# Performance work log

Measured on AMD Instinct MI355X. Metric: run time of the kernel, lower is better.

Reference implementation:

```python
import jax, jax.numpy as jnp
import numpy as np

# Object condensation loss config (matches init_kwargs / HGCalML defaults)
Q_MIN = 0.5
S_B = 1.0
POT_SCALE = 1.0
REP_SCALE = 1.0
BETA_SCALE = 1.0
E_WEIGHT = 1.0
HUBER_DELTA = 2.0
E_DEN_OFFSET = 1.0
K_MAX = 192          # object-id slots per event; id 0 = noise
EPS = 1e-6

B, N = 4, 50000


def setup_inputs() -> dict:
    key = jax.random.key(0)
    k1, k2, k3, k4, k5 = jax.random.split(key, 5)
    return {
        "beta": jax.random.uniform(k1, (B, N, 1), dtype=jnp.float32),
        "ccoords": jax.random.normal(k2, (B, N, 2), dtype=jnp.float32),
        "pred_energy": jax.random.uniform(k3, (B, N, 1), dtype=jnp.float32),
        "true_energy": jax.random.uniform(k4, (B, N, 1), dtype=jnp.float32),
        "truth_idx": jax.random.randint(k5, (B, N), 0, K_MAX, dtype=jnp.int32),
    }


def _per_event(beta, ccoords, pred_e, true_e, tidx):
    # beta: [N,1], ccoords: [N,2], tidx: [N] int (0 = noise)
    beta = jnp.clip(beta[:, 0], 1e-4, 1.0 - 1e-4)            # [N]
    q = jnp.arctanh(beta) ** 2 + Q_MIN                        # charge  [N]

    ids = jnp.arange(K_MAX)
    M = (tidx[:, None] == ids[None, :]) & (ids[None, :] > 0)  # [N,K] membership
    Mf = M.astype(q.dtype)
    obj_valid = jnp.any(M, axis=0)                            # [K]
    vf = obj_valid.astype(q.dtype)

    # condensation point alpha_k = argmax_q over members of object k
    qM = jnp.where(M, q[:, None], -1.0)                       # [N,K]
    idx_alpha = jnp.argmax(qM, axis=0)                        # [K]
    x_alpha = ccoords[idx_alpha]                              # [K,2]
    q_alpha = q[idx_alpha]                                    # [K]
    beta_alpha = beta[idx_alpha]                              # [K]

    # pairwise hit<->condensation-point distances
    d2 = jnp.sum((ccoords[:, None, :] - x_alpha[None, :, :]) ** 2, axis=-1)  # [N,K]

    # attractive potential (members), repulsive hinge (non-members of valid objects)
    att = jnp.sum(d2 * q_alpha[None, :] * Mf, axis=-1)                       # [N]
    dist = jnp.sqrt(d2 + EPS)
    rep = jnp.sum(jnp.maximum(0.0, 1.0 - dist) * q_alpha[None, :]
                  * (1.0 - Mf) * vf[None, :], axis=-1)                       # [N]
    L_V = jnp.mean(q * (POT_SCALE * att + REP_SCALE * rep))

    n_obj = jnp.sum(vf) + EPS
    L_beta = BETA_SCALE * jnp.sum((1.0 - beta_alpha) * vf) / n_obj

    noise = (tidx == 0).astype(q.dtype)
    L_noise = S_B * jnp.sum(beta * noise) / (jnp.sum(noise) + EPS)

    # energy payload loss: relative error, Huber, beta-weighted per object
    ediff = (pred_e[:, 0] - true_e[:, 0]) / (true_e[:, 0] + E_DEN_OFFSET)
    ad = jnp.abs(ediff)
    eh = jnp.where(ad <= HUBER_DELTA, 0.5 * ad ** 2,
                   HUBER_DELTA * (ad - 0.5 * HUBER_DELTA))                   # [N]
    pw = Mf * beta[:, None]                                                  # [N,K]
    per_obj_e = jnp.sum(pw * eh[:, None], axis=0) / (jnp.sum(pw, axis=0) + EPS)
    L_E = E_WEIGHT * jnp.sum(per_obj_e * vf) / n_obj

    return L_V + L_beta + L_noise + L_E


def reference(beta, ccoords, pred_energy, true_energy, truth_idx):
    per_ev = jax.vmap(_per_event)(beta, ccoords, pred_energy, true_energy, truth_idx)
    return jnp.mean(per_ev)
```

## Files before the change

kernel.cpp:

```cpp
#include <hip/hip_runtime.h>
#include <math.h>

#define KM 192
#define EPSF 1e-6f
#define QMIN 0.5f
#define BLKA 256
#define HA 4
#define TILEA (BLKA * HA)
#define BLKM 256
#define TILEM (BLKM * 2)

__device__ __forceinline__ float clipb(float b) {
    return fminf(fmaxf(b, 1e-4f), 1.0f - 1e-4f);
}
__device__ __forceinline__ float fast_atanh(float b) {
    float r = (1.f + b) * __builtin_amdgcn_rcpf(1.f - b);
    return 0.34657359f * __builtin_amdgcn_logf(r);
}

__global__ void __launch_bounds__(BLKA)
k_amax(const float* __restrict__ beta, const int* __restrict__ tidx,
       unsigned long long* __restrict__ pscr, int N, int HBT) {
    const int e = blockIdx.y;
    __shared__ unsigned long long smax[KM];
    for (int k = threadIdx.x; k < KM; k += BLKA) smax[k] = 0ull;
    __syncthreads();
    const size_t base = (size_t)e * N;
    #pragma unroll
    for (int h = 0; h < HA; ++h) {
        int i = blockIdx.x * TILEA + h * BLKA + threadIdx.x;
        if (i < N) {
            int t = tidx[base + i];
            if (t > 0) {
                float bc = clipb(beta[base + i]);
                unsigned long long pack =
                    ((unsigned long long)__float_as_uint(bc) << 32) |
                    (unsigned long long)(unsigned)(N - 1 - i);
                atomicMax(&smax[t], pack);
            }
        }
    }
    __syncthreads();
    unsigned long long* row = pscr + ((size_t)e * HBT + blockIdx.x) * KM;
    for (int k = threadIdx.x; k < KM; k += BLKA) row[k] = smax[k];
}

__global__ void __launch_bounds__(256)
k_alpha(const unsigned long long* __restrict__ pscr, const float* __restrict__ cc,
        float4* __restrict__ alpha, float* __restrict__ abw,
        float* __restrict__ enm, float* __restrict__ eden,
        float* __restrict__ scal, int N, int HBT) {
    const int e = blockIdx.x;
    const int k = threadIdx.x;
    if (k < KM) {
        const unsigned long long* pk = pscr + (size_t)e * HBT * KM + k;
        unsigned long long v = 0ull;
        #pragma unroll 8
        for (int t = 0; t < HBT; ++t) {
            unsigned long long p = pk[(size_t)t * KM];
            if (p > v) v = p;
        }
        float4 a = make_float4(0.f, 0.f, 0.f, 0.f);
        float bw = 0.f;
        if (v) {
            int idx = N - 1 - (int)(unsigned)(v & 0xffffffffull);
            bw = __uint_as_float((unsigned)(v >> 32));
            float at = fast_atanh(bw);
            float2 cp = ((const float2*)cc)[(size_t)e * N + idx];
            a.x = cp.x; a.y = cp.y;
            a.z = fmaf(at, at, QMIN);
        }
        alpha[e * KM + k] = a;
        abw  [e * KM + k] = bw;
    }
    for (int z = threadIdx.x; z < KM; z += 256) {
        enm [e * KM + z] = 0.f;
        eden[e * KM + z] = 0.f;
    }
    if (threadIdx.x < 8) scal[e * 8 + threadIdx.x] = 0.f;
}

__global__ void __launch_bounds__(BLKM, 4)
k_main(const float* __restrict__ beta, const float* __restrict__ cc,
       const float* __restrict__ pe,   const float* __restrict__ te,
       const int* __restrict__ tidx,   const float4* __restrict__ alpha,
       float* __restrict__ enm, float* __restrict__ eden,
       float* __restrict__ scal, int N) {
    const int e = blockIdx.y;
    __shared__ float sn[KM], sd[KM];
    __shared__ float sw[12];
    for (int k = threadIdx.x; k < KM; k += BLKM) { sn[k] = 0.f; sd[k] = 0.f; }
    __syncthreads();

    const size_t base = (size_t)e * N;
    const int ia = blockIdx.x * TILEM + threadIdx.x;
    const int ib = ia + BLKM;
    const bool oka = ia < N, okb = ib < N;
    const size_t iia = base + (oka ? ia : 0);
    const size_t iib = base + (okb ? ib : 0);
    const float2 ca = ((const float2*)cc)[iia];
    const float2 cb = ((const float2*)cc)[iib];
    const float bca = clipb(beta[iia]);
    const float bcb = clipb(beta[iib]);
    const int   ta  = oka ? tidx[iia] : 0;
    const int   tb  = okb ? tidx[iib] : 0;
    const float ha_ = fast_atanh(bca);
    const float hb_ = fast_atanh(bcb);
    const float qa  = oka ? fmaf(ha_, ha_, QMIN) : 0.f;
    const float qb  = okb ? fmaf(hb_, hb_, QMIN) : 0.f;

    const float4* __restrict__ ae = alpha + e * KM;
    float ra0 = 0.f, ra1 = 0.f, rb0 = 0.f, rb1 = 0.f;
    #pragma unroll 8
    for (int k = 0; k < KM; k += 2) {
        float4 a0 = ae[k], a1 = ae[k + 1];
        float dxa0 = ca.x - a0.x, dya0 = ca.y - a0.y;
        float dxa1 = ca.x - a1.x, dya1 = ca.y - a1.y;
        float dxb0 = cb.x - a0.x, dyb0 = cb.y - a0.y;
        float dxb1 = cb.x - a1.x, dyb1 = cb.y - a1.y;
        float da0 = fmaf(dxa0, dxa0, fmaf(dya0, dya0, EPSF));
        float da1 = fmaf(dxa1, dxa1, fmaf(dya1, dya1, EPSF));
        float db0 = fmaf(dxb0, dxb0, fmaf(dyb0, dyb0, EPSF));
        float db1 = fmaf(dxb1, dxb1, fmaf(dyb1, dyb1, EPSF));
        ra0 = fmaf(fmaxf(1.f - __builtin_amdgcn_sqrtf(da0), 0.f), a0.z, ra0);
        ra1 = fmaf(fmaxf(1.f - __builtin_amdgcn_sqrtf(da1), 0.f), a1.z, ra1);
        rb0 = fmaf(fmaxf(1.f - __builtin_amdgcn_sqrtf(db0), 0.f), a0.z, rb0);
        rb1 = fmaf(fmaxf(1.f - __builtin_amdgcn_sqrtf(db1), 0.f), a1.z, rb1);
    }
    float repa = ra0 + ra1, repb = rb0 + rb1;
    float atta = 0.f, attb = 0.f, bn = 0.f, cn = 0.f;

    if (ta > 0) {
        float4 av = ae[ta];
        float dx = ca.x - av.x, dy = ca.y - av.y;
        float d2 = fmaf(dx, dx, dy * dy);
        atta = d2 * av.z;
        repa -= fmaxf(1.f - __builtin_amdgcn_sqrtf(d2 + EPSF), 0.f) * av.z;
        float tev = te[iia];
        float edv = (pe[iia] - tev) * __builtin_amdgcn_rcpf(tev + 1.f);
        float ad  = fabsf(edv);
        float eh  = (ad <= 2.f) ? 0.5f * ad * ad : 2.f * (ad - 1.f);
        atomicAdd(&sn[ta], bca * eh);
        atomicAdd(&sd[ta], bca);
    } else if (oka) { bn += bca; cn += 1.f; }

    if (tb > 0) {
        float4 av = ae[tb];
        float dx = cb.x - av.x, dy = cb.y - av.y;
        float d2 = fmaf(dx, dx, dy * dy);
        attb = d2 * av.z;
        repb -= fmaxf(1.f - __builtin_amdgcn_sqrtf(d2 + EPSF), 0.f) * av.z;
        float tev = te[iib];
        float edv = (pe[iib] - tev) * __builtin_amdgcn_rcpf(tev + 1.f);
        float ad  = fabsf(edv);
        float eh  = (ad <= 2.f) ? 0.5f * ad * ad : 2.f * (ad - 1.f);
        atomicAdd(&sn[tb], bcb * eh);
        atomicAdd(&sd[tb], bcb);
    } else if (okb) { bn += bcb; cn += 1.f; }

    float lv = fmaf(qa, atta + repa, qb * (attb + repb));
    __syncthreads();

    if (threadIdx.x < KM) {
        float vd = sd[threadIdx.x];
        if (vd != 0.f) {
            atomicAdd(&enm [e * KM + threadIdx.x], sn[threadIdx.x]);
            atomicAdd(&eden[e * KM + threadIdx.x], vd);
        }
    }
    for (int off = 32; off > 0; off >>= 1) {
        lv += __shfl_down(lv, off);
        bn += __shfl_down(bn, off);
        cn += __shfl_down(cn, off);
    }
    const int wid = threadIdx.x >> 6;
    if ((threadIdx.x & 63) == 0) { sw[wid] = lv; sw[4 + wid] = bn; sw[8 + wid] = cn; }
    __syncthreads();
    if (threadIdx.x == 0) {
        atomicAdd(&scal[e * 8 + 0], (sw[0] + sw[1]) + (sw[2] + sw[3]));
        atomicAdd(&scal[e * 8 + 3], (sw[4] + sw[5]) + (sw[6] + sw[7]));
        atomicAdd(&scal[e * 8 + 4], (sw[8] + sw[9]) + (sw[10] + sw[11]));
    }
}

__global__ void __launch_bounds__(256)
k_fin(const float* __restrict__ enm, const float* __restrict__ eden,
      const float* __restrict__ abw, const float* __restrict__ scal,
      float* __restrict__ out, int N, int B) {
    __shared__ float sred[12];
    const int wid = threadIdx.x >> 6;
    float tot = 0.f;
    for (int ev = 0; ev < B; ++ev) {
        float lb = 0.f, nv = 0.f, le = 0.f;
        if (threadIdx.x < KM) {
            float bw = abw[ev * KM + threadIdx.x];
            if (bw > 0.f) {
                lb = 1.f - bw;
                nv = 1.f;
                le = enm[ev * KM + threadIdx.x] / (eden[ev * KM + threadIdx.x] + EPSF);
            }
        }
        for (int off = 32; off > 0; off >>= 1) {
            lb += __shfl_down(lb, off);
            nv += __shfl_down(nv, off);
            le += __shfl_down(le, off);
        }
        if ((threadIdx.x & 63) == 0) { sred[wid] = lb; sred[4 + wid] = nv; sred[8 + wid] = le; }
        __syncthreads();
        if (threadIdx.x == 0) {
            float lbs = (sred[0] + sred[1]) + (sred[2] + sred[3]);
            float nvs = (sred[4] + sred[5]) + (sred[6] + sred[7]);
            float les = (sred[8] + sred[9]) + (sred[10] + sred[11]);
            float nobj = nvs + EPSF;
            tot += scal[ev * 8 + 0] / (float)N + lbs / nobj
                 + scal[ev * 8 + 3] / (scal[ev * 8 + 4] + EPSF) + les / nobj;
        }
        __syncthreads();
    }
    if (threadIdx.x == 0) out[0] = tot / (float)B;
}

extern "C" void kernel_launch(void* const* d_in, const int* in_sizes, int n_in,
                              void* d_out, int out_size, void* d_ws, size_t ws_size,
                              hipStream_t stream) {
    const int B = 4;
    const int N = in_sizes[0] / B;
    const int HBT = (N + TILEA - 1) / TILEA;
    const int MB  = (N + TILEM - 1) / TILEM;

    const float* beta = (const float*)d_in[0];
    const float* cc   = (const float*)d_in[1];
    const float* pe   = (const float*)d_in[2];
    const float* te   = (const float*)d_in[3];
    const int*   tidx = (const int*)  d_in[4];
    float* out = (float*)d_out;

    char* ws = (char*)d_ws;
    unsigned long long* pscr = (unsigned long long*)ws;
    float4* alpha = (float4*)(ws + (size_t)B * HBT * KM * 8);
    float*  abw   = (float*)(alpha + B * KM);
    float*  enm   = abw  + B * KM;
    float*  eden  = enm  + B * KM;
    float*  scal  = eden + B * KM;

    k_amax<<<dim3(HBT, B), dim3(BLKA), 0, stream>>>(beta, tidx, pscr, N, HBT);
    k_alpha<<<dim3(B), dim3(256), 0, stream>>>(pscr, cc, alpha, abw, enm, eden, scal, N, HBT);
    k_main<<<dim3(MB, B), dim3(BLKM), 0, stream>>>(
        beta, cc, pe, te, tidx, alpha, enm, eden, scal, N);
    k_fin<<<dim3(1), dim3(256), 0, stream>>>(enm, eden, abw, scal, out, N, B);
}
```

Baseline: 99.99 us.

## Keep condensation points in registers and broadcast hits via readlane in repulsion loop

Reorganizes the repulsion computation so each lane owns three of the 192 condensation points in registers, while hit coordinates and charges are broadcast across the wavefront with readlane. This removes the per-iteration loads of the alpha array (float4 per object per hit pair). The grid changes to a fixed 128 tiles per event, with each block looping over its strided hits. The q_alpha weighting is applied once at the end. The cost is a serialized readlane per hit and fewer blocks (512 total), which may lower occupancy. Per-hit bookkeeping and atomics are unchanged.

Measured after the change: 102.7 us. 1.03x slower.

```diff
diff --git a/kernel.cpp b/kernel.cpp
--- a/kernel.cpp
+++ b/kernel.cpp
@@ -8,7 +8,7 @@
 #define HA 4
 #define TILEA (BLKA * HA)
 #define BLKM 256
-#define TILEM (BLKM * 2)
+#define NTILES 128
 
 __device__ __forceinline__ float clipb(float b) {
     return fminf(fmaxf(b, 1e-4f), 1.0f - 1e-4f);
@@ -16,6 +16,9 @@
 __device__ __forceinline__ float fast_atanh(float b) {
     float r = (1.f + b) * __builtin_amdgcn_rcpf(1.f - b);
     return 0.34657359f * __builtin_amdgcn_logf(r);
+}
+__device__ __forceinline__ float bcast(float v, int j) {
+    return __int_as_float(__builtin_amdgcn_readlane(__float_as_int(v), j));
 }
 
 __global__ void __launch_bounds__(BLKA)
@@ -87,78 +90,68 @@
        float* __restrict__ enm, float* __restrict__ eden,
        float* __restrict__ scal, int N) {
     const int e = blockIdx.y;
+    const int lane = threadIdx.x & 63;
     __shared__ float sn[KM], sd[KM];
     __shared__ float sw[12];
     for (int k = threadIdx.x; k < KM; k += BLKM) { sn[k] = 0.f; sd[k] = 0.f; }
+
+    const float4* __restrict__ ae = alpha + e * KM;
+    const float4 o0 = ae[lane];
+    const float4 o1 = ae[lane + 64];
+    const float4 o2 = ae[lane + 128];
     __syncthreads();
 
     const size_t base = (size_t)e * N;
-    const int ia = blockIdx.x * TILEM + threadIdx.x;
-    const int ib = ia + BLKM;
-    const bool oka = ia < N, okb = ib < N;
-    const size_t iia = base + (oka ? ia : 0);
-    const size_t iib = base + (okb ? ib : 0);
-    const float2 ca = ((const float2*)cc)[iia];
-    const float2 cb = ((const float2*)cc)[iib];
-    const float bca = clipb(beta[iia]);
-    const float bcb = clipb(beta[iib]);
-    const int   ta  = oka ? tidx[iia] : 0;
-    const int   tb  = okb ? tidx[iib] : 0;
-    const float ha_ = fast_atanh(bca);
-    const float hb_ = fast_atanh(bcb);
-    const float qa  = oka ? fmaf(ha_, ha_, QMIN) : 0.f;
-    const float qb  = okb ? fmaf(hb_, hb_, QMIN) : 0.f;
-
-    const float4* __restrict__ ae = alpha + e * KM;
-    float ra0 = 0.f, ra1 = 0.f, rb0 = 0.f, rb1 = 0.f;
-    #pragma unroll 8
-    for (int k = 0; k < KM; k += 2) {
-        float4 a0 = ae[k], a1 = ae[k + 1];
-        float dxa0 = ca.x - a0.x, dya0 = ca.y - a0.y;
-        float dxa1 = ca.x - a1.x, dya1 = ca.y - a1.y;
-        float dxb0 = cb.x - a0.x, dyb0 = cb.y - a0.y;
-        float dxb1 = cb.x - a1.x, dyb1 = cb.y - a1.y;
-        float da0 = fmaf(dxa0, dxa0, fmaf(dya0, dya0, EPSF));
-        float da1 = fmaf(dxa1, dxa1, fmaf(dya1, dya1, EPSF));
-        float db0 = fmaf(dxb0, dxb0, fmaf(dyb0, dyb0, EPSF));
-        float db1 = fmaf(dxb1, dxb1, fmaf(dyb1, dyb1, EPSF));
-        ra0 = fmaf(fmaxf(1.f - __builtin_amdgcn_sqrtf(da0), 0.f), a0.z, ra0);
-        ra1 = fmaf(fmaxf(1.f - __builtin_amdgcn_sqrtf(da1), 0.f), a1.z, ra1);
-        rb0 = fmaf(fmaxf(1.f - __builtin_amdgcn_sqrtf(db0), 0.f), a0.z, rb0);
-        rb1 = fmaf(fmaxf(1.f - __builtin_amdgcn_sqrtf(db1), 0.f), a1.z, rb1);
-    }
-    float repa = ra0 + ra1, repb = rb0 + rb1;
-    float atta = 0.f, attb = 0.f, bn = 0.f, cn = 0.f;
-
-    if (ta > 0) {
-        float4 av = ae[ta];
-        float dx = ca.x - av.x, dy = ca.y - av.y;
-        float d2 = fmaf(dx, dx, dy * dy);
-        atta = d2 * av.z;
-        repa -= fmaxf(1.f - __builtin_amdgcn_sqrtf(d2 + EPSF), 0.f) * av.z;
-        float tev = te[iia];
-        float edv = (pe[iia] - tev) * __builtin_amdgcn_rcpf(tev + 1.f);
-        float ad  = fabsf(edv);
-        float eh  = (ad <= 2.f) ? 0.5f * ad * ad : 2.f * (ad - 1.f);
-        atomicAdd(&sn[ta], bca * eh);
-        atomicAdd(&sd[ta], bca);
-    } else if (oka) { bn += bca; cn += 1.f; }
-
-    if (tb > 0) {
-        float4 av = ae[tb];
-        float dx = cb.x - av.x, dy = cb.y - av.y;
-        float d2 = fmaf(dx, dx, dy * dy);
-        attb = d2 * av.z;
-        repb -= fmaxf(1.f - __builtin_amdgcn_sqrtf(d2 + EPSF), 0.f) * av.z;
-        float tev = te[iib];
-        float edv = (pe[iib] - tev) * __builtin_amdgcn_rcpf(tev + 1.f);
-        float ad  = fabsf(edv);
-        float eh  = (ad <= 2.f) ? 0.5f * ad * ad : 2.f * (ad - 1.f);
-        atomicAdd(&sn[tb], bcb * eh);
-        atomicAdd(&sd[tb], bcb);
-    } else if (okb) { bn += bcb; cn += 1.f; }
-
-    float lv = fmaf(qa, atta + repa, qb * (attb + repb));
+    const int hpt   = (N + NTILES - 1) / NTILES;
+    const int start = blockIdx.x * hpt;
+    const int end   = min(start + hpt, N);
+    const int nst   = (hpt + BLKM - 1) / BLKM;
+
+    float r0 = 0.f, r1 = 0.f, r2 = 0.f;
+    float lvh = 0.f, bn = 0.f, cn = 0.f;
+
+    for (int s = 0; s < nst; ++s) {
+        const int i = start + s * BLKM + (int)threadIdx.x;
+        const bool ok = i < end;
+        const size_t ii = base + (ok ? i : 0);
+        const float2 cp = ((const float2*)cc)[ii];
+        const float  bc = clipb(beta[ii]);
+        const int    t  = ok ? tidx[ii] : -1;
+        const float  at = fast_atanh(bc);
+        const float  qh = ok ? fmaf(at, at, QMIN) : 0.f;
+
+        if (t > 0) {
+            float4 av = ae[t];
+            float dx = cp.x - av.x, dy = cp.y - av.y;
+            float d2 = fmaf(dx, dx, dy * dy);
+            float hin = fmaxf(1.f - __builtin_amdgcn_sqrtf(d2 + EPSF), 0.f);
+            lvh = fmaf(qh * av.z, d2 - hin, lvh);
+            float tev = te[ii];
+            float edv = (pe[ii] - tev) * __builtin_amdgcn_rcpf(tev + 1.f);
+            float ad  = fabsf(edv);
+            float eh  = (ad <= 2.f) ? 0.5f * ad * ad : 2.f * (ad - 1.f);
+            atomicAdd(&sn[t], bc * eh);
+            atomicAdd(&sd[t], bc);
+        } else if (t == 0) { bn += bc; cn += 1.f; }
+
+        #pragma unroll 16
+        for (int j = 0; j < 64; ++j) {
+            const float xh = bcast(cp.x, j);
+            const float yh = bcast(cp.y, j);
+            const float qb = bcast(qh,  j);
+            float dx0 = o0.x - xh, dy0 = o0.y - yh;
+            float dx1 = o1.x - xh, dy1 = o1.y - yh;
+            float dx2 = o2.x - xh, dy2 = o2.y - yh;
+            float d0 = fmaf(dx0, dx0, fmaf(dy0, dy0, EPSF));
+            float d1 = fmaf(dx1, dx1, fmaf(dy1, dy1, EPSF));
+            float d2 = fmaf(dx2, dx2, fmaf(dy2, dy2, EPSF));
+            r0 = fmaf(fmaxf(1.f - __builtin_amdgcn_sqrtf(d0), 0.f), qb, r0);
+            r1 = fmaf(fmaxf(1.f - __builtin_amdgcn_sqrtf(d1), 0.f), qb, r1);
+            r2 = fmaf(fmaxf(1.f - __builtin_amdgcn_sqrtf(d2), 0.f), qb, r2);
+        }
+    }
+
+    float lv = fmaf(o0.z, r0, fmaf(o1.z, r1, fmaf(o2.z, r2, lvh)));
     __syncthreads();
 
     if (threadIdx.x < KM) {
@@ -226,7 +219,6 @@
     const int B = 4;
     const int N = in_sizes[0] / B;
     const int HBT = (N + TILEA - 1) / TILEA;
-    const int MB  = (N + TILEM - 1) / TILEM;
 
     const float* beta = (const float*)d_in[0];
     const float* cc   = (const float*)d_in[1];
@@ -245,7 +237,7 @@
 
     k_amax<<<dim3(HBT, B), dim3(BLKA), 0, stream>>>(beta, tidx, pscr, N, HBT);
     k_alpha<<<dim3(B), dim3(256), 0, stream>>>(pscr, cc, alpha, abw, enm, eden, scal, N, HBT);
-    k_main<<<dim3(MB, B), dim3(BLKM), 0, stream>>>(
+    k_main<<<dim3(NTILES, B), dim3(BLKM), 0, stream>>>(
         beta, cc, pe, te, tidx, alpha, enm, eden, scal, N);
     k_fin<<<dim3(1), dim3(256), 0, stream>>>(enm, eden, abw, scal, out, N, B);
 }
```
